# Optimization experiments

Hardware: AMD Instinct MI355X
Metric: run time of the kernel (lower is better)

Reference implementation:

```python
import jax, jax.numpy as jnp
import numpy as np

N = 100000   # nodes
E = 1600000  # edges
G = 512      # graphs
IN_F = 128
HID = 64
EPS = 1e-5


def setup_inputs() -> dict:
    key = jax.random.key(0)
    ks = jax.random.split(key, 16)
    x = jax.random.normal(ks[0], (N, IN_F), dtype=jnp.float32)
    edge_index = jax.random.randint(ks[1], (2, E), 0, N, dtype=jnp.int64)
    batch = jnp.sort(jax.random.randint(ks[2], (N,), 0, G, dtype=jnp.int64))
    s = 0.05
    return {
        'x': x, 'edge_index': edge_index, 'batch': batch,
        'W1': jax.random.normal(ks[3], (IN_F, HID), jnp.float32) * s,
        'b1': jax.random.normal(ks[4], (HID,), jnp.float32) * s,
        'g1': jax.random.uniform(ks[5], (HID,), jnp.float32),
        'be1': jax.random.normal(ks[6], (HID,), jnp.float32) * s,
        'rm1': jnp.zeros((HID,), jnp.float32),
        'rv1': jnp.ones((HID,), jnp.float32),
        'W2': jax.random.normal(ks[7], (HID, HID), jnp.float32) * s,
        'b2': jax.random.normal(ks[8], (HID,), jnp.float32) * s,
        'g2': jax.random.uniform(ks[9], (HID,), jnp.float32),
        'be2': jax.random.normal(ks[10], (HID,), jnp.float32) * s,
        'rm2': jnp.zeros((HID,), jnp.float32),
        'rv2': jnp.ones((HID,), jnp.float32),
        'Wh1': jax.random.normal(ks[11], (2 * HID, HID), jnp.float32) * s,
        'bh1': jax.random.normal(ks[12], (HID,), jnp.float32) * s,
        'Wh2': jax.random.normal(ks[13], (HID, HID // 2), jnp.float32) * s,
        'bh2': jnp.zeros((HID // 2,), jnp.float32),
        'Wh3': jax.random.normal(ks[14], (HID // 2, 1), jnp.float32) * s,
        'bh3': jnp.zeros((1,), jnp.float32),
    }


def _gcn(h, W, b, src, dst):
    # GCNConv with added self-loops and symmetric D^{-1/2} A D^{-1/2} normalization
    hw = h @ W                                   # [N, HID]
    deg = jnp.ones((N,), hw.dtype).at[dst].add(1.0)  # in-degree + self-loop
    dinv = jax.lax.rsqrt(deg)
    norm = dinv[src] * dinv[dst]                 # [E]
    agg = jax.ops.segment_sum(hw[src] * norm[:, None], dst, num_segments=N)
    return agg + hw * (dinv * dinv)[:, None] + b  # self-loop term + bias


def _bn(x, g, b, rm, rv):
    return (x - rm) * jax.lax.rsqrt(rv + EPS) * g + b


def reference(x, edge_index, batch, W1, b1, g1, be1, rm1, rv1,
              W2, b2, g2, be2, rm2, rv2, Wh1, bh1, Wh2, bh2, Wh3, bh3):
    src, dst = edge_index[0], edge_index[1]
    # layer 0 (no residual: dim change 128 -> 64)
    h = jax.nn.relu(_bn(_gcn(x, W1, b1, src, dst), g1, be1, rm1, rv1))
    # layer 1 with residual
    h = h + jax.nn.relu(_bn(_gcn(h, W2, b2, src, dst), g2, be2, rm2, rv2))
    # global mean + max pooling per graph
    ones = jnp.ones((N,), h.dtype)
    cnt = jnp.maximum(jax.ops.segment_sum(ones, batch, num_segments=G), 1.0)
    h_mean = jax.ops.segment_sum(h, batch, num_segments=G) / cnt[:, None]
    h_max = jax.ops.segment_max(h, batch, num_segments=G)
    hg = jnp.concatenate([h_mean, h_max], axis=-1)   # [G, 2*HID]
    # MLP head (dropout disabled in eval)
    z = jax.nn.relu(hg @ Wh1 + bh1)
    z = jax.nn.relu(z @ Wh2 + bh2)
    out = z @ Wh3 + bh3
    return jax.nn.sigmoid(out).squeeze(-1)           # [G]
```

## Files before the change

### kernel.cpp

```cpp
#include <hip/hip_runtime.h>
#include <math.h>

#define NN 100000
#define EE 1600000
#define GG 512
#define INF_ 128
#define HID 64
#define EPS 1e-5f

#define NBUK 391
#define P1_TILES 98
#define SETUP_B 25
#define POOL_WORDS (GG * 64 * 2 + GG)
#define ZERO_B ((POOL_WORDS + 255) / 256)

typedef unsigned int uint32;
typedef __attribute__((ext_vector_type(8))) short bf16x8;
typedef __attribute__((ext_vector_type(4))) float f32x4;

static __device__ inline uint32 f2bf(float f) {
    uint32 u = __float_as_uint(f);
    return (u + 0x7FFFu + ((u >> 16) & 1u)) >> 16;
}
static __device__ inline float bf_lo(uint32 u) { return __uint_as_float(u << 16); }
static __device__ inline float bf_hi(uint32 u) { return __uint_as_float(u & 0xFFFF0000u); }



__global__ __launch_bounds__(256) void k_hist1(const int* __restrict__ ei,
        int* __restrict__ hblk,
        const float* b1, const float* g1, const float* be1,
        const float* rm1, const float* rv1,
        const float* b2, const float* g2, const float* be2,
        const float* rm2, const float* rv2, float* sc,
        const float* W1, uint32* Wt1b, const float* W2, uint32* Wt2b,
        uint32* hwb, float* poolz) {
    int b = blockIdx.x, t = threadIdx.x;
    if (b < P1_TILES) {
        __shared__ int h[NBUK];
        for (int i = t; i < NBUK; i += 256) h[i] = 0;
        __syncthreads();
        const int4* dst4 = (const int4*)(ei + EE);
        int base4 = b * 4096;
        for (int j = 0; j < 16; ++j) {
            int i4 = base4 + j * 256 + t;
            if (i4 < EE / 4) {
                int4 d = dst4[i4];
                atomicAdd(&h[d.x >> 8], 1);
                atomicAdd(&h[d.y >> 8], 1);
                atomicAdd(&h[d.z >> 8], 1);
                atomicAdd(&h[d.w >> 8], 1);
            }
        }
        __syncthreads();
        for (int i = t; i < NBUK; i += 256) hblk[i * P1_TILES + b] = h[i];
    } else if (b < P1_TILES + SETUP_B) {
        int i = (b - P1_TILES) * 256 + t;
        if (i < 4096) {
            int n = i >> 6, kp = (i & 63) * 2;
            Wt1b[i] = f2bf(W1[(size_t)kp * 64 + n]) |
                      (f2bf(W1[(size_t)(kp + 1) * 64 + n]) << 16);
        } else if (i < 6144) {
            int j = i - 4096;
            int n = j >> 5, kp = (j & 31) * 2;
            Wt2b[j] = f2bf(W2[(size_t)kp * 64 + n]) |
                      (f2bf(W2[(size_t)(kp + 1) * 64 + n]) << 16);
        } else if (i < 6208) {
            int l = i - 6144;
            float s1 = g1[l] * rsqrtf(rv1[l] + EPS);
            sc[l]       = s1;
            sc[64 + l]  = (b1[l] - rm1[l]) * s1 + be1[l];
            float s2 = g2[l] * rsqrtf(rv2[l] + EPS);
            sc[128 + l] = s2;
            sc[192 + l] = (b2[l] - rm2[l]) * s2 + be2[l];
        } else if (i < 6240) {
            hwb[(size_t)NN * 32 + (i - 6208)] = 0u;
        }
    } else {
        int i = (b - P1_TILES - SETUP_B) * 256 + t;
        if (i < POOL_WORDS) poolz[i] = 0.f;
    }
}

__global__ void k_scan2(const int* __restrict__ hblk, int* __restrict__ bbase,
                        int* __restrict__ rbase, int* __restrict__ offs) {
    __shared__ int wsum[8];
    int t = threadIdx.x;
    int lane = t & 63, w = t >> 6;
    int c = 0;
    if (t < NBUK)
        for (int b = 0; b < P1_TILES; ++b) c += hblk[t * P1_TILES + b];
    int v = c;
    for (int d = 1; d < 64; d <<= 1) { int n = __shfl_up(v, d); if (lane >= d) v += n; }
    if (lane == 63) wsum[w] = v;
    __syncthreads();
    int pre = 0;
    for (int q = 0; q < w; ++q) pre += wsum[q];
    int excl = pre + v - c;
    if (t <= NBUK) bbase[t] = excl;
    if (t == 0) offs[NN] = EE;
    if (t < NBUK) {
        int run = excl;
        for (int b = 0; b < P1_TILES; ++b) {
            rbase[t * P1_TILES + b] = run;
            run += hblk[t * P1_TILES + b];
        }
    }
}

__global__ __launch_bounds__(256) void k_p1b(const int* __restrict__ ei,
                                             const int* __restrict__ rbase,
                                             uint32* __restrict__ pairs) {
    __shared__ int h[NBUK];
    int b = blockIdx.x, t = threadIdx.x;
    for (int i = t; i < NBUK; i += 256) h[i] = rbase[i * P1_TILES + b];
    __syncthreads();
    const int4* src4 = (const int4*)ei;
    const int4* dst4 = (const int4*)(ei + EE);
    int base4 = b * 4096;
    for (int j = 0; j < 16; ++j) {
        int i4 = base4 + j * 256 + t;
        if (i4 < EE / 4) {
            int4 d = dst4[i4];
            int4 s = src4[i4];
            int p0 = atomicAdd(&h[d.x >> 8], 1);
            pairs[p0] = ((uint32)s.x << 8) | (uint32)(d.x & 255);
            int p1 = atomicAdd(&h[d.y >> 8], 1);
            pairs[p1] = ((uint32)s.y << 8) | (uint32)(d.y & 255);
            int p2 = atomicAdd(&h[d.z >> 8], 1);
            pairs[p2] = ((uint32)s.z << 8) | (uint32)(d.z & 255);
            int p3 = atomicAdd(&h[d.w >> 8], 1);
            pairs[p3] = ((uint32)s.w << 8) | (uint32)(d.w & 255);
        }
    }
}

__global__ __launch_bounds__(256) void k_p2(const uint32* __restrict__ pairs,
                                            const int* __restrict__ bbase,
                                            int* __restrict__ offs, float* __restrict__ dinv,
                                            int* __restrict__ col) {
    int b = blockIdx.x, t = threadIdx.x;
    int nbase = b << 8;
    int ebase = bbase[b], eend = bbase[b + 1];
    int m = eend - ebase;
    __shared__ int cnt[256];
    __shared__ int wsum[4];
    cnt[t] = 0;
    __syncthreads();
    for (int i = t; i < m; i += 256)
        atomicAdd(&cnt[pairs[ebase + i] & 255u], 1);
    __syncthreads();
    int c = cnt[t];
    int lane = t & 63, w = t >> 6;
    int v = c;
    for (int d = 1; d < 64; d <<= 1) { int n = __shfl_up(v, d); if (lane >= d) v += n; }
    if (lane == 63) wsum[w] = v;
    __syncthreads();
    int pre = 0;
    for (int q = 0; q < w; ++q) pre += wsum[q];
    int excl = pre + v - c;
    int node = nbase + t;
    if (node < NN) {
        offs[node] = ebase + excl;
        dinv[node] = rsqrtf(1.f + (float)c);
    }
    __syncthreads();
    cnt[t] = excl;
    __syncthreads();
    for (int i = t; i < m; i += 256) {
        uint32 u = pairs[ebase + i];
        int loc = atomicAdd(&cnt[u & 255u], 1);
        col[ebase + loc] = (int)(u >> 8);
    }
}

template <int K, int XBF16>
__global__ __launch_bounds__(256) void k_gemm_mfma(const void* __restrict__ Xv,
                                                   const uint32* __restrict__ Wtb,
                                                   const float* __restrict__ dinv,
                                                   uint32* __restrict__ outb, int nrows) {
    constexpr int KP = K + 8;
    __shared__ alignas(16) unsigned short Al[64 * KP];
    __shared__ alignas(16) unsigned short Bl[64 * KP];
    int tid = threadIdx.x;
    for (int i = tid; i < 64 * (K / 2); i += 256) {
        int n = i / (K / 2), kp = i % (K / 2);
        *(uint32*)&Bl[n * KP + kp * 2] = Wtb[i];
    }
    int r0 = blockIdx.x * 64;
    if (XBF16 == 0) {
        const float* Xb = (const float*)Xv + (size_t)r0 * K;
        int limit = (nrows - r0) * K;
        for (int f = tid * 4; f < 64 * K; f += 1024) {
            float4 v = {0.f, 0.f, 0.f, 0.f};
            if (f + 3 < limit) v = *(const float4*)&Xb[f];
            int row = f / K, kpos = f % K;
            ushort4 pk;
            pk.x = (unsigned short)f2bf(v.x);
            pk.y = (unsigned short)f2bf(v.y);
            pk.z = (unsigned short)f2bf(v.z);
            pk.w = (unsigned short)f2bf(v.w);
            *(ushort4*)&Al[row * KP + kpos] = pk;
        }
    } else {
        const uint32* Xb = (const uint32*)Xv;
        for (int i = tid; i < 64 * (K / 2); i += 256) {
            int row = i / (K / 2), c = i % (K / 2);
            uint32 v = 0;
            if (r0 + row < nrows) v = Xb[(size_t)(r0 + row) * (K / 2) + c];
            *(uint32*)&Al[row * KP + 2 * c] = v;
        }
    }
    __syncthreads();
    int lane = tid & 63, wv = tid >> 6;
    int m = lane & 15, quad = lane >> 4;
    f32x4 acc0 = {0.f, 0.f, 0.f, 0.f}, acc1 = acc0, acc2 = acc0, acc3 = acc0;
    int arow = wv * 16 + m;
#pragma unroll
    for (int k0 = 0; k0 < K; k0 += 32) {
        int koff = k0 + quad * 8;
        bf16x8 a = *(const bf16x8*)&Al[arow * KP + koff];
        bf16x8 b0 = *(const bf16x8*)&Bl[(0 * 16 + m) * KP + koff];
        bf16x8 b1 = *(const bf16x8*)&Bl[(1 * 16 + m) * KP + koff];
        bf16x8 b2 = *(const bf16x8*)&Bl[(2 * 16 + m) * KP + koff];
        bf16x8 b3 = *(const bf16x8*)&Bl[(3 * 16 + m) * KP + koff];
        acc0 = __builtin_amdgcn_mfma_f32_16x16x32_bf16(a, b0, acc0, 0, 0, 0);
        acc1 = __builtin_amdgcn_mfma_f32_16x16x32_bf16(a, b1, acc1, 0, 0, 0);
        acc2 = __builtin_amdgcn_mfma_f32_16x16x32_bf16(a, b2, acc2, 0, 0, 0);
        acc3 = __builtin_amdgcn_mfma_f32_16x16x32_bf16(a, b3, acc3, 0, 0, 0);
    }
    float dsc[4];
#pragma unroll
    for (int reg = 0; reg < 4; ++reg) {
        int row = r0 + wv * 16 + quad * 4 + reg;
        dsc[reg] = (row < nrows) ? dinv[row] : 0.f;
    }
    const float* accs[4] = {(const float*)&acc0, (const float*)&acc1,
                            (const float*)&acc2, (const float*)&acc3};
#pragma unroll
    for (int nt = 0; nt < 4; ++nt) {
#pragma unroll
        for (int reg = 0; reg < 4; ++reg) {
            float val = accs[nt][reg] * dsc[reg];
            float nxt = __shfl_down(val, 1);
            int row = r0 + wv * 16 + quad * 4 + reg;
            if (((m & 1) == 0) && row < nrows)
                outb[(size_t)row * 32 + nt * 8 + (m >> 1)] =
                    f2bf(val) | (f2bf(nxt) << 16);
        }
    }
}

__global__ void k_gcn_gather(const uint32* __restrict__ hwb, const int* __restrict__ col,
                             const int* __restrict__ offs,
                             const float* __restrict__ dinv, const float* __restrict__ scale,
                             const float* __restrict__ shift, const uint32* __restrict__ resid,
                             uint32* __restrict__ outb) {
    int node = blockIdx.x * 4 + (threadIdx.x >> 6);
    if (node >= NN) return;
    int lane = threadIdx.x & 63;
    int half = lane >> 5;
    int fl = lane & 31;
    int e0 = offs[node], e1 = offs[node + 1];
    float di = dinv[node];
    float ax0 = 0.f, ay0 = 0.f, ax1 = 0.f, ay1 = 0.f;
    for (int base = e0; base < e1; base += 64) {
        int m = e1 - base; if (m > 64) m = 64;
        int srcv = NN;
        if (lane < m) srcv = col[base + lane];
        for (int j = 0; j < m; j += 16) {
            int s0 = __shfl(srcv, j + half);
            int s1 = __shfl(srcv, j + 2 + half);
            int s2 = __shfl(srcv, j + 4 + half);
            int s3 = __shfl(srcv, j + 6 + half);
            int s4 = __shfl(srcv, j + 8 + half);
            int s5 = __shfl(srcv, j + 10 + half);
            int s6 = __shfl(srcv, j + 12 + half);
            int s7 = __shfl(srcv, j + 14 + half);
            uint32 u0 = hwb[(size_t)s0 * 32 + fl];
            uint32 u1 = hwb[(size_t)s1 * 32 + fl];
            uint32 u2 = hwb[(size_t)s2 * 32 + fl];
            uint32 u3 = hwb[(size_t)s3 * 32 + fl];
            uint32 u4 = hwb[(size_t)s4 * 32 + fl];
            uint32 u5 = hwb[(size_t)s5 * 32 + fl];
            uint32 u6 = hwb[(size_t)s6 * 32 + fl];
            uint32 u7 = hwb[(size_t)s7 * 32 + fl];
            ax0 += bf_lo(u0); ay0 += bf_hi(u0);
            ax1 += bf_lo(u1); ay1 += bf_hi(u1);
            ax0 += bf_lo(u2); ay0 += bf_hi(u2);
            ax1 += bf_lo(u3); ay1 += bf_hi(u3);
            ax0 += bf_lo(u4); ay0 += bf_hi(u4);
            ax1 += bf_lo(u5); ay1 += bf_hi(u5);
            ax0 += bf_lo(u6); ay0 += bf_hi(u6);
            ax1 += bf_lo(u7); ay1 += bf_hi(u7);
        }
    }
    float ax = ax0 + ax1, ay = ay0 + ay1;
    ax += __shfl(ax, fl + 32);
    ay += __shfl(ay, fl + 32);
    if (half == 0) {
        uint32 uself = hwb[(size_t)node * 32 + fl];
        ax += bf_lo(uself); ay += bf_hi(uself);
        float vx = fmaf(ax * di, scale[2 * fl],     shift[2 * fl]);
        float vy = fmaf(ay * di, scale[2 * fl + 1], shift[2 * fl + 1]);
        vx = fmaxf(vx, 0.f);
        vy = fmaxf(vy, 0.f);
        if (resid) {
            uint32 rv = resid[(size_t)node * 32 + fl];
            vx += bf_lo(rv); vy += bf_hi(rv);
        }
        outb[(size_t)node * 32 + fl] = f2bf(vx) | (f2bf(vy) << 16);
    }
}

__global__ __launch_bounds__(256) void k_pool(const uint32* __restrict__ hb,
                       const int* __restrict__ batch,
                       float* __restrict__ msum, float* __restrict__ mmax,
                       float* __restrict__ gcnt) {
    int l = threadIdx.x & 31;
    int hf = threadIdx.x >> 5;
    int i0 = blockIdx.x * 256 + hf * 32;
    if (i0 >= NN) return;
    int i1 = i0 + 32; if (i1 > NN) i1 = NN;
    int cur = batch[i0];
    float s0 = 0.f, s1 = 0.f, m0 = 0.f, m1 = 0.f; int c = 0;
    for (int i = i0; i < i1; ++i) {
        int g = batch[i];
        if (g != cur) {
            atomicAdd(&msum[cur * 64 + 2 * l], s0);
            atomicAdd(&msum[cur * 64 + 2 * l + 1], s1);
            atomicMax((unsigned int*)&mmax[cur * 64 + 2 * l], __float_as_uint(m0));
            atomicMax((unsigned int*)&mmax[cur * 64 + 2 * l + 1], __float_as_uint(m1));
            if (l == 0) atomicAdd(&gcnt[cur], (float)c);
            s0 = s1 = m0 = m1 = 0.f; c = 0; cur = g;
        }
        uint32 u = hb[(size_t)i * 32 + l];
        float vx = bf_lo(u), vy = bf_hi(u);
        s0 += vx; s1 += vy; m0 = fmaxf(m0, vx); m1 = fmaxf(m1, vy); ++c;
    }
    atomicAdd(&msum[cur * 64 + 2 * l], s0);
    atomicAdd(&msum[cur * 64 + 2 * l + 1], s1);
    atomicMax((unsigned int*)&mmax[cur * 64 + 2 * l], __float_as_uint(m0));
    atomicMax((unsigned int*)&mmax[cur * 64 + 2 * l + 1], __float_as_uint(m1));
    if (l == 0) atomicAdd(&gcnt[cur], (float)c);
}

__global__ void k_head(const float* __restrict__ msum, const float* __restrict__ mmax,
                       const float* __restrict__ gcnt,
                       const float* __restrict__ Wh1, const float* __restrict__ bh1,
                       const float* __restrict__ Wh2, const float* __restrict__ bh2,
                       const float* __restrict__ Wh3, const float* __restrict__ bh3,
                       float* __restrict__ out) {
    int g = blockIdx.x, t = threadIdx.x;
    __shared__ float hg[128];
    __shared__ float z1[64];
    __shared__ float z2[32];
    float c = fmaxf(gcnt[g], 1.f);
    hg[t]      = msum[g * 64 + t] / c;
    hg[64 + t] = mmax[g * 64 + t];
    __syncthreads();
    float acc = bh1[t];
#pragma unroll 8
    for (int k = 0; k < 128; ++k) acc = fmaf(hg[k], Wh1[k * 64 + t], acc);
    z1[t] = fmaxf(acc, 0.f);
    __syncthreads();
    if (t < 32) {
        float a2 = bh2[t];
#pragma unroll 8
        for (int k = 0; k < 64; ++k) a2 = fmaf(z1[k], Wh2[k * 32 + t], a2);
        z2[t] = fmaxf(a2, 0.f);
    }
    __syncthreads();
    if (t == 0) {
        float a3 = bh3[0];
        for (int k = 0; k < 32; ++k) a3 = fmaf(z2[k], Wh3[k], a3);
        out[g] = 1.f / (1.f + expf(-a3));
    }
}


static inline size_t alignup(size_t x) { return (x + 255) & ~(size_t)255; }

extern "C" void kernel_launch(void* const* d_in, const int* in_sizes, int n_in,
                              void* d_out, int out_size, void* d_ws, size_t ws_size,
                              hipStream_t stream) {
    const float* x   = (const float*)d_in[0];
    const int*   ei  = (const int*)d_in[1];
    const int*   bat = (const int*)d_in[2];
    const float* W1  = (const float*)d_in[3];
    const float* b1  = (const float*)d_in[4];
    const float* g1  = (const float*)d_in[5];
    const float* be1 = (const float*)d_in[6];
    const float* rm1 = (const float*)d_in[7];
    const float* rv1 = (const float*)d_in[8];
    const float* W2  = (const float*)d_in[9];
    const float* b2  = (const float*)d_in[10];
    const float* g2  = (const float*)d_in[11];
    const float* be2 = (const float*)d_in[12];
    const float* rm2 = (const float*)d_in[13];
    const float* rv2 = (const float*)d_in[14];
    const float* Wh1 = (const float*)d_in[15];
    const float* bh1 = (const float*)d_in[16];
    const float* Wh2 = (const float*)d_in[17];
    const float* bh2 = (const float*)d_in[18];
    const float* Wh3 = (const float*)d_in[19];
    const float* bh3 = (const float*)d_in[20];
    float* out = (float*)d_out;

    char* ws = (char*)d_ws;
    size_t o = 0;
    int*   hblk   = (int*)(ws + o);  o = alignup(o + (size_t)P1_TILES * NBUK * 4);
    int*   rbase  = (int*)(ws + o);  o = alignup(o + (size_t)P1_TILES * NBUK * 4);
    int*   bbase  = (int*)(ws + o);  o = alignup(o + (NBUK + 1) * 4);
    int*   offs   = (int*)(ws + o);  o = alignup(o + (NN + 1) * 4);
    uint32* pairs = (uint32*)(ws + o); o = alignup(o + (size_t)EE * 4);
    int*   col    = (int*)(ws + o);  o = alignup(o + (size_t)EE * 4);
    float* dinv   = (float*)(ws + o); o = alignup(o + (size_t)NN * 4);
    float* scb    = (float*)(ws + o); o = alignup(o + 4 * 64 * 4);
    uint32* Wt1b  = (uint32*)(ws + o); o = alignup(o + 64 * (INF_ / 2) * 4);
    uint32* Wt2b  = (uint32*)(ws + o); o = alignup(o + 64 * (HID / 2) * 4);
    float* msum   = (float*)(ws + o); o += (size_t)GG * 64 * 4;
    float* mmax   = (float*)(ws + o); o += (size_t)GG * 64 * 4;
    float* gcnt   = (float*)(ws + o); o += (size_t)GG * 4;
    o = alignup(o);
    uint32* hwb   = (uint32*)(ws + o); o = alignup(o + ((size_t)NN + 1) * 32 * 4);
    uint32* hb    = (uint32*)(ws + o); o = alignup(o + (size_t)NN * 32 * 4);
    (void)ws_size; (void)n_in; (void)in_sizes; (void)out_size;

    k_hist1<<<P1_TILES + SETUP_B + ZERO_B, 256, 0, stream>>>(
        ei, hblk, b1, g1, be1, rm1, rv1, b2, g2, be2, rm2, rv2, scb,
        W1, Wt1b, W2, Wt2b, hwb, msum);
    k_scan2<<<1, 512, 0, stream>>>(hblk, bbase, rbase, offs);
    k_p1b<<<P1_TILES, 256, 0, stream>>>(ei, rbase, pairs);
    k_p2<<<NBUK, 256, 0, stream>>>(pairs, bbase, offs, dinv, col);

    k_gemm_mfma<INF_, 0><<<(NN + 63) / 64, 256, 0, stream>>>(x, Wt1b, dinv, hwb, NN);
    k_gcn_gather<<<(NN + 3) / 4, 256, 0, stream>>>(hwb, col, offs, dinv,
                                                   scb, scb + 64, nullptr, hb);
    k_gemm_mfma<HID, 1><<<(NN + 63) / 64, 256, 0, stream>>>(hb, Wt2b, dinv, hwb, NN);
    k_gcn_gather<<<(NN + 3) / 4, 256, 0, stream>>>(hwb, col, offs, dinv,
                                                   scb + 128, scb + 192, hb, hb);
    k_pool<<<(NN + 255) / 256, 256, 0, stream>>>(hb, bat, msum, mmax, gcnt);
    k_head<<<GG, 64, 0, stream>>>(msum, mmax, gcnt, Wh1, bh1, Wh2, bh2, Wh3, bh3, out);
}
```

Measured before the change: 317.0 us.

## Stage CSR bucket scatter and column fill in shared memory for coalesced writes

The edge-tile count is doubled, so each of the 196 tiles now handles 8192 edges. k_p1b buckets each tile into an LDS staging buffer using a local prefix scan, then copies each bucket contiguously to global memory instead of scattering one word at a time. k_p2 loads its bucket's pairs into LDS, builds the col array there, and writes it back coalesced, falling back to global memory past a 5120-entry cap. The goal is to cut scattered global writes during CSR construction, at the cost of large LDS use (about 34 KB and 41 KB per block), which lowers occupancy, plus a longer serial scan in k_scan2.

```diff
diff --git a/kernel.cpp b/kernel.cpp
--- a/kernel.cpp
+++ b/kernel.cpp
@@ -9,10 +9,11 @@
 #define EPS 1e-5f
 
 #define NBUK 391
-#define P1_TILES 98
+#define P1T 196
 #define SETUP_B 25
 #define POOL_WORDS (GG * 64 * 2 + GG)
 #define ZERO_B ((POOL_WORDS + 255) / 256)
+#define P2CAP 5120
 
 typedef unsigned int uint32;
 typedef __attribute__((ext_vector_type(8))) short bf16x8;
@@ -24,7 +25,6 @@
 }
 static __device__ inline float bf_lo(uint32 u) { return __uint_as_float(u << 16); }
 static __device__ inline float bf_hi(uint32 u) { return __uint_as_float(u & 0xFFFF0000u); }
-
 
 
 __global__ __launch_bounds__(256) void k_hist1(const int* __restrict__ ei,
@@ -36,13 +36,13 @@
         const float* W1, uint32* Wt1b, const float* W2, uint32* Wt2b,
         uint32* hwb, float* poolz) {
     int b = blockIdx.x, t = threadIdx.x;
-    if (b < P1_TILES) {
+    if (b < P1T) {
         __shared__ int h[NBUK];
         for (int i = t; i < NBUK; i += 256) h[i] = 0;
         __syncthreads();
         const int4* dst4 = (const int4*)(ei + EE);
-        int base4 = b * 4096;
-        for (int j = 0; j < 16; ++j) {
+        int base4 = b * 2048;
+        for (int j = 0; j < 8; ++j) {
             int i4 = base4 + j * 256 + t;
             if (i4 < EE / 4) {
                 int4 d = dst4[i4];
@@ -53,9 +53,9 @@
             }
         }
         __syncthreads();
-        for (int i = t; i < NBUK; i += 256) hblk[i * P1_TILES + b] = h[i];
-    } else if (b < P1_TILES + SETUP_B) {
-        int i = (b - P1_TILES) * 256 + t;
+        for (int i = t; i < NBUK; i += 256) hblk[i * P1T + b] = h[i];
+    } else if (b < P1T + SETUP_B) {
+        int i = (b - P1T) * 256 + t;
         if (i < 4096) {
             int n = i >> 6, kp = (i & 63) * 2;
             Wt1b[i] = f2bf(W1[(size_t)kp * 64 + n]) |
@@ -77,7 +77,7 @@
             hwb[(size_t)NN * 32 + (i - 6208)] = 0u;
         }
     } else {
-        int i = (b - P1_TILES - SETUP_B) * 256 + t;
+        int i = (b - P1T - SETUP_B) * 256 + t;
         if (i < POOL_WORDS) poolz[i] = 0.f;
     }
 }
@@ -89,7 +89,7 @@
     int lane = t & 63, w = t >> 6;
     int c = 0;
     if (t < NBUK)
-        for (int b = 0; b < P1_TILES; ++b) c += hblk[t * P1_TILES + b];
+        for (int b = 0; b < P1T; ++b) c += hblk[t * P1T + b];
     int v = c;
     for (int d = 1; d < 64; d <<= 1) { int n = __shfl_up(v, d); if (lane >= d) v += n; }
     if (lane == 63) wsum[w] = v;
@@ -101,37 +101,67 @@
     if (t == 0) offs[NN] = EE;
     if (t < NBUK) {
         int run = excl;
-        for (int b = 0; b < P1_TILES; ++b) {
-            rbase[t * P1_TILES + b] = run;
-            run += hblk[t * P1_TILES + b];
+        for (int b = 0; b < P1T; ++b) {
+            rbase[t * P1T + b] = run;
+            run += hblk[t * P1T + b];
         }
     }
 }
 
 __global__ __launch_bounds__(256) void k_p1b(const int* __restrict__ ei,
+                                             const int* __restrict__ hblk,
                                              const int* __restrict__ rbase,
                                              uint32* __restrict__ pairs) {
-    __shared__ int h[NBUK];
+    __shared__ uint32 stage[8192];
+    __shared__ int hloc[NBUK];
+    __shared__ int lbase[NBUK];
+    __shared__ int cur[NBUK];
+    __shared__ int wsum[4];
     int b = blockIdx.x, t = threadIdx.x;
-    for (int i = t; i < NBUK; i += 256) h[i] = rbase[i * P1_TILES + b];
-    __syncthreads();
+    int lane = t & 63, w = t >> 6;
+    for (int i = t; i < NBUK; i += 256) hloc[i] = hblk[i * P1T + b];
+    __syncthreads();
+    int carry = 0;
+    for (int r = 0; r < 2; ++r) {
+        int idx = r * 256 + t;
+        int c = (idx < NBUK) ? hloc[idx] : 0;
+        int v = c;
+        for (int d = 1; d < 64; d <<= 1) { int n = __shfl_up(v, d); if (lane >= d) v += n; }
+        if (lane == 63) wsum[w] = v;
+        __syncthreads();
+        int pre = 0;
+        for (int q = 0; q < w; ++q) pre += wsum[q];
+        int excl = pre + v - c + carry;
+        if (idx < NBUK) { lbase[idx] = excl; cur[idx] = excl; }
+        carry += wsum[0] + wsum[1] + wsum[2] + wsum[3];
+        __syncthreads();
+    }
     const int4* src4 = (const int4*)ei;
     const int4* dst4 = (const int4*)(ei + EE);
-    int base4 = b * 4096;
-    for (int j = 0; j < 16; ++j) {
+    int base4 = b * 2048;
+    for (int j = 0; j < 8; ++j) {
         int i4 = base4 + j * 256 + t;
         if (i4 < EE / 4) {
             int4 d = dst4[i4];
             int4 s = src4[i4];
-            int p0 = atomicAdd(&h[d.x >> 8], 1);
-            pairs[p0] = ((uint32)s.x << 8) | (uint32)(d.x & 255);
-            int p1 = atomicAdd(&h[d.y >> 8], 1);
-            pairs[p1] = ((uint32)s.y << 8) | (uint32)(d.y & 255);
-            int p2 = atomicAdd(&h[d.z >> 8], 1);
-            pairs[p2] = ((uint32)s.z << 8) | (uint32)(d.z & 255);
-            int p3 = atomicAdd(&h[d.w >> 8], 1);
-            pairs[p3] = ((uint32)s.w << 8) | (uint32)(d.w & 255);
-        }
+            int p0 = atomicAdd(&cur[d.x >> 8], 1);
+            stage[p0] = ((uint32)s.x << 8) | (uint32)(d.x & 255);
+            int p1 = atomicAdd(&cur[d.y >> 8], 1);
+            stage[p1] = ((uint32)s.y << 8) | (uint32)(d.y & 255);
+            int p2 = atomicAdd(&cur[d.z >> 8], 1);
+            stage[p2] = ((uint32)s.z << 8) | (uint32)(d.z & 255);
+            int p3 = atomicAdd(&cur[d.w >> 8], 1);
+            stage[p3] = ((uint32)s.w << 8) | (uint32)(d.w & 255);
+        }
+    }
+    __syncthreads();
+    for (int k = w; k < NBUK; k += 4) {
+        int len = hloc[k];
+        if (!len) continue;
+        int gdst = rbase[k * P1T + b];
+        int lsrc = lbase[k];
+        for (int i = lane; i < len; i += 64)
+            pairs[gdst + i] = stage[lsrc + i];
     }
 }
 
@@ -139,16 +169,20 @@
                                             const int* __restrict__ bbase,
                                             int* __restrict__ offs, float* __restrict__ dinv,
                                             int* __restrict__ col) {
+    __shared__ uint32 pL[P2CAP];
+    __shared__ int colL[P2CAP];
+    __shared__ int cnt[256];
+    __shared__ int wsum[4];
     int b = blockIdx.x, t = threadIdx.x;
     int nbase = b << 8;
     int ebase = bbase[b], eend = bbase[b + 1];
     int m = eend - ebase;
-    __shared__ int cnt[256];
-    __shared__ int wsum[4];
+    int mm = m < P2CAP ? m : P2CAP;
+    for (int i = t; i < mm; i += 256) pL[i] = pairs[ebase + i];
     cnt[t] = 0;
     __syncthreads();
-    for (int i = t; i < m; i += 256)
-        atomicAdd(&cnt[pairs[ebase + i] & 255u], 1);
+    for (int i = t; i < mm; i += 256) atomicAdd(&cnt[pL[i] & 255u], 1);
+    for (int i = P2CAP + t; i < m; i += 256) atomicAdd(&cnt[pairs[ebase + i] & 255u], 1);
     __syncthreads();
     int c = cnt[t];
     int lane = t & 63, w = t >> 6;
@@ -167,11 +201,20 @@
     __syncthreads();
     cnt[t] = excl;
     __syncthreads();
-    for (int i = t; i < m; i += 256) {
+    for (int i = t; i < mm; i += 256) {
+        uint32 u = pL[i];
+        int loc = atomicAdd(&cnt[u & 255u], 1);
+        if (loc < P2CAP) colL[loc] = (int)(u >> 8);
+        else col[ebase + loc] = (int)(u >> 8);
+    }
+    for (int i = P2CAP + t; i < m; i += 256) {
         uint32 u = pairs[ebase + i];
         int loc = atomicAdd(&cnt[u & 255u], 1);
-        col[ebase + loc] = (int)(u >> 8);
-    }
+        if (loc < P2CAP) colL[loc] = (int)(u >> 8);
+        else col[ebase + loc] = (int)(u >> 8);
+    }
+    __syncthreads();
+    for (int i = t; i < mm; i += 256) col[ebase + i] = colL[i];
 }
 
 template <int K, int XBF16>
@@ -409,8 +452,8 @@
 
     char* ws = (char*)d_ws;
     size_t o = 0;
-    int*   hblk   = (int*)(ws + o);  o = alignup(o + (size_t)P1_TILES * NBUK * 4);
-    int*   rbase  = (int*)(ws + o);  o = alignup(o + (size_t)P1_TILES * NBUK * 4);
+    int*   hblk   = (int*)(ws + o);  o = alignup(o + (size_t)P1T * NBUK * 4);
+    int*   rbase  = (int*)(ws + o);  o = alignup(o + (size_t)P1T * NBUK * 4);
     int*   bbase  = (int*)(ws + o);  o = alignup(o + (NBUK + 1) * 4);
     int*   offs   = (int*)(ws + o);  o = alignup(o + (NN + 1) * 4);
     uint32* pairs = (uint32*)(ws + o); o = alignup(o + (size_t)EE * 4);
@@ -427,11 +470,11 @@
     uint32* hb    = (uint32*)(ws + o); o = alignup(o + (size_t)NN * 32 * 4);
     (void)ws_size; (void)n_in; (void)in_sizes; (void)out_size;
 
-    k_hist1<<<P1_TILES + SETUP_B + ZERO_B, 256, 0, stream>>>(
+    k_hist1<<<P1T + SETUP_B + ZERO_B, 256, 0, stream>>>(
         ei, hblk, b1, g1, be1, rm1, rv1, b2, g2, be2, rm2, rv2, scb,
         W1, Wt1b, W2, Wt2b, hwb, msum);
     k_scan2<<<1, 512, 0, stream>>>(hblk, bbase, rbase, offs);
-    k_p1b<<<P1_TILES, 256, 0, stream>>>(ei, rbase, pairs);
+    k_p1b<<<P1T, 256, 0, stream>>>(ei, hblk, rbase, pairs);
     k_p2<<<NBUK, 256, 0, stream>>>(pairs, bbase, offs, dinv, col);
 
     k_gemm_mfma<INF_, 0><<<(NN + 63) / 64, 256, 0, stream>>>(x, Wt1b, dinv, hwb, NN);
```

New measurement: 350.3 us. 1.1x slower.
